# Kernel optimization log

Measured on AMD Instinct MI355X. Metric: run time of the kernel, lower is better.

Reference implementation:

```python
import jax, jax.numpy as jnp
import numpy as np

B, S, H = 2, 1024, 2048
HQ, HKV, D = 16, 4, 128
E, K, CAP = 32, 4, 512
IM, SIM = 512, 1024
EPS = 1e-6
THETA = 1.0e6
T = B * S


def setup_inputs() -> dict:
    key = jax.random.key(0)
    ks = jax.random.split(key, 16)
    r = lambda i, shape, s=0.02: jax.random.normal(ks[i], shape, dtype=jnp.float32) * s
    return {
        "hidden_states": jax.random.normal(ks[0], (T, H), dtype=jnp.float32),
        "positions": jnp.tile(jnp.arange(S, dtype=jnp.int32), B),
        "ln1_w": jnp.ones((H,), jnp.float32),
        "ln2_w": jnp.ones((H,), jnp.float32),
        "wq": r(1, (H, HQ * D)),
        "wk": r(2, (H, HKV * D)),
        "wv": r(3, (H, HKV * D)),
        "wo": r(4, (HQ * D, H)),
        "qn_w": jnp.ones((D,), jnp.float32),
        "kn_w": jnp.ones((D,), jnp.float32),
        "gate_w": r(5, (H, E), 0.05),
        "expert_bias": r(6, (E,), 0.1),
        "w_gate_e": r(7, (E, H, IM)),
        "w_up_e": r(8, (E, H, IM)),
        "w_down_e": r(9, (E, IM, H)),
        "ws_gate": r(10, (H, SIM)),
        "ws_up": r(11, (H, SIM)),
        "ws_down": r(12, (SIM, H)),
    }


def _rms(x, w):
    return x * jax.lax.rsqrt(jnp.mean(x * x, axis=-1, keepdims=True) + EPS) * w


def _forward(hidden_states, positions, ln1_w, ln2_w, wq, wk, wv, wo, qn_w, kn_w,
             gate_w, expert_bias, w_gate_e, w_up_e, w_down_e, ws_gate, ws_up, ws_down):
    # --- attention block ---
    resid = hidden_states
    h = _rms(hidden_states, ln1_w)
    q = (h @ wq).reshape(T, HQ, D)
    k = (h @ wk).reshape(T, HKV, D)
    v = (h @ wv).reshape(T, HKV, D)
    q = _rms(q, qn_w)  # per-head qk-norm
    k = _rms(k, kn_w)
    # neox-style RoPE over full head_dim
    inv = 1.0 / (THETA ** (jnp.arange(0, D, 2, dtype=jnp.float32) / D))
    fr = positions.astype(jnp.float32)[:, None] * inv  # [T, D/2]
    cos, sin = jnp.cos(fr)[:, None, :], jnp.sin(fr)[:, None, :]
    def rope(x):
        x1, x2 = jnp.split(x, 2, axis=-1)
        return jnp.concatenate([x1 * cos - x2 * sin, x2 * cos + x1 * sin], axis=-1)
    q, k = rope(q), rope(k)
    qb = q.reshape(B, S, HQ, D)
    kb = jnp.repeat(k.reshape(B, S, HKV, D), HQ // HKV, axis=2)  # GQA expand
    vb = jnp.repeat(v.reshape(B, S, HKV, D), HQ // HKV, axis=2)
    sc = jnp.einsum('bqhd,bkhd->bhqk', qb, kb) * (D ** -0.5)
    causal = jnp.tril(jnp.ones((S, S), dtype=bool))
    sc = jnp.where(causal, sc, jnp.float32(-1e30))
    p = jax.nn.softmax(sc, axis=-1)
    ao = jnp.einsum('bhqk,bkhd->bqhd', p, vb).reshape(T, HQ * D)
    h = ao @ wo + resid
    resid = h
    h = _rms(h, ln2_w)
    # --- shared experts (dense MLP) ---
    shared = (jax.nn.silu(h @ ws_gate) * (h @ ws_up)) @ ws_down
    # --- sigmoid router with correction bias (bias only for selection) ---
    scores = jax.nn.sigmoid(h @ gate_w)          # [T, E]
    _, idx = jax.lax.top_k(scores + expert_bias, K)
    w = jnp.take_along_axis(scores, idx, axis=-1)
    w = w / jnp.sum(w, axis=-1, keepdims=True)   # renormalize top-k probs
    # --- capacity-based dispatch / grouped GEMM / combine ---
    flat_e = idx.reshape(-1)                     # [T*K]
    flat_t = jnp.repeat(jnp.arange(T), K)
    flat_w = w.reshape(-1)
    order = jnp.argsort(flat_e)                  # stable sort by expert
    se, st, sw = flat_e[order], flat_t[order], flat_w[order]
    counts = jnp.bincount(flat_e, length=E)
    starts = jnp.concatenate([jnp.zeros((1,), counts.dtype), jnp.cumsum(counts)[:-1]])
    pos = jnp.arange(T * K) - starts[se]         # slot within expert
    valid = pos < CAP                            # capacity guard (never trips in practice)
    posc = jnp.minimum(pos, CAP - 1)
    xbuf = jnp.zeros((E, CAP, H), h.dtype).at[se, posc].add(
        jnp.where(valid[:, None], h[st], 0.0))   # [E, CAP, H]
    inter = jax.nn.silu(jnp.einsum('ech,ehi->eci', xbuf, w_gate_e)) \
            * jnp.einsum('ech,ehi->eci', xbuf, w_up_e)
    obuf = jnp.einsum('eci,eih->ech', inter, w_down_e)
    y = obuf[se, posc] * jnp.where(valid, sw, 0.0)[:, None]
    moe = jnp.zeros((T, H), h.dtype).at[st].add(y)
    return resid + moe + shared


def reference(hidden_states, positions, ln1_w, ln2_w, wq, wk, wv, wo, qn_w, kn_w,
              gate_w, expert_bias, w_gate_e, w_up_e, w_down_e, ws_gate, ws_up, ws_down):
    return _forward(hidden_states, positions, ln1_w, ln2_w, wq, wk, wv, wo, qn_w, kn_w,
                    gate_w, expert_bias, w_gate_e, w_up_e, w_down_e, ws_gate, ws_up, ws_down)
```

## Files before the change

### kernel.cpp

```cpp
#include <hip/hip_runtime.h>
#include <stdint.h>

typedef unsigned short u16;
typedef unsigned short bf16u;
typedef unsigned int u32;
typedef _Float16 f16;
typedef __attribute__((ext_vector_type(8))) short bf16x8;
typedef __attribute__((ext_vector_type(8))) _Float16 f16x8;
typedef __attribute__((ext_vector_type(4))) float f32x4;

#define T_N 2048
#define H_N 2048
#define S_N 1024
#define B_N 2
#define HQ_N 16
#define HKV_N 4
#define D_N 128
#define E_N 32
#define K_TOP 4
#define CAP_N 512
#define IM_N 512
#define SIM_N 1024
#define QD_N 2048
#define KD_N 512
#define QKV_N 3072
#define NFLAT (T_N*K_TOP)
#define RGRP 128
#define NGRP (NFLAT/RGRP)

#define SC_H1   1024.0f
#define SC_W    512.0f
#define SC_QK   2048.0f
#define SC_P    4096.0f
#define SC_V    2048.0f
#define OSC_QKV (1.0f/524288.0f)
#define OSC_OPJ (1.0f/1048576.0f)

__device__ __forceinline__ float bf2f(bf16u x){ return __uint_as_float(((u32)x)<<16); }
__device__ __forceinline__ bf16u f2bf(float f){
  u32 u = __float_as_uint(f);
  u32 r = (u + 0x7FFFu + ((u>>16)&1u)) >> 16;
  return (bf16u)r;
}
__device__ __forceinline__ u32 pkbf(float a, float b){
  u32 ua = __float_as_uint(a), ub = __float_as_uint(b);
  u32 ra = (ua + 0x7FFFu + ((ua>>16)&1u)) >> 16;
  u32 rb = (ub + 0x7FFFu + ((ub>>16)&1u)) & 0xFFFF0000u;
  return ra | rb;
}
__device__ __forceinline__ void split2h(float x, u16& h, u16& l){
  f16 hh = (f16)x;
  f16 ll = (f16)(x - (float)hh);
  h = __builtin_bit_cast(u16, hh);
  l = __builtin_bit_cast(u16, ll);
}
__device__ __forceinline__ f32x4 mfma16b(bf16x8 a, bf16x8 b, f32x4 c){
  return __builtin_amdgcn_mfma_f32_16x16x32_bf16(a,b,c,0,0,0);
}
__device__ __forceinline__ f32x4 mfma16h(f16x8 a, f16x8 b, f32x4 c){
  return __builtin_amdgcn_mfma_f32_16x16x32_f16(a,b,c,0,0,0);
}
__device__ __forceinline__ void gl_lds16(const void* g, void* l){
  __builtin_amdgcn_global_load_lds((const __attribute__((address_space(1))) u32*)g,
                                   (__attribute__((address_space(3))) u32*)l, 16, 0, 0);
}
__device__ __forceinline__ int xcd_swz(int lin, int nwg){
  int cpx = nwg >> 3;
  return (lin & 7)*cpx + (lin >> 3);
}

__global__ __launch_bounds__(256) void transpose_f32(const float* __restrict__ in,
                                                     float* __restrict__ out, int R, int C){
  __shared__ float tile[32][33];
  int rb = blockIdx.x*32, cb = blockIdx.y*32;
  int tx = threadIdx.x, ty = threadIdx.y;
  #pragma unroll
  for (int kk=0;kk<4;kk++)
    tile[ty+kk*8][tx] = in[(size_t)(rb+ty+kk*8)*C + cb + tx];
  __syncthreads();
  #pragma unroll
  for (int kk=0;kk<4;kk++)
    out[(size_t)(cb+ty+kk*8)*R + rb + tx] = tile[tx][ty+kk*8];
}

__global__ __launch_bounds__(256) void transpose_cvt_g(const float* __restrict__ in,
                                                       bf16u* __restrict__ out, int R, int C){
  __shared__ float tile[64*64];
  size_t zo = (size_t)blockIdx.z * R * C;
  int rb = blockIdx.x*64, cb = blockIdx.y*64;
  int tid = threadIdx.x, wave = tid>>6, lane = tid&63;
  #pragma unroll
  for (int p=0;p<4;p++){
    int r = p*16 + wave*4 + (lane>>4);
    const float* src = in + zo + (size_t)(rb + r)*C + cb + (lane&15)*4;
    gl_lds16(src, &tile[(p*16 + wave*4)*64]);
  }
  __syncthreads();
  int c = tid>>2, rq = (tid&3)*16;
  u16 tmp[16];
  #pragma unroll
  for (int j=0;j<16;j++) tmp[j] = f2bf(tile[(rq+j)*64 + c]);
  uint4 w0, w1;
  w0.x=(u32)tmp[0]|((u32)tmp[1]<<16);  w0.y=(u32)tmp[2]|((u32)tmp[3]<<16);
  w0.z=(u32)tmp[4]|((u32)tmp[5]<<16);  w0.w=(u32)tmp[6]|((u32)tmp[7]<<16);
  w1.x=(u32)tmp[8]|((u32)tmp[9]<<16);  w1.y=(u32)tmp[10]|((u32)tmp[11]<<16);
  w1.z=(u32)tmp[12]|((u32)tmp[13]<<16); w1.w=(u32)tmp[14]|((u32)tmp[15]<<16);
  bf16u* dst = out + zo + (size_t)(cb+c)*R + rb + rq;
  *(uint4*)dst = w0;
  *(uint4*)(dst+8) = w1;
}

__global__ __launch_bounds__(256) void transpose_split16_g(const float* __restrict__ in,
                                                           u16* __restrict__ oh,
                                                           u16* __restrict__ ol,
                                                           int R, int C, float scale){
  __shared__ float tile[64*64];
  int rb = blockIdx.x*64, cb = blockIdx.y*64;
  int tid = threadIdx.x, wave = tid>>6, lane = tid&63;
  #pragma unroll
  for (int p=0;p<4;p++){
    int r = p*16 + wave*4 + (lane>>4);
    const float* src = in + (size_t)(rb + r)*C + cb + (lane&15)*4;
    gl_lds16(src, &tile[(p*16 + wave*4)*64]);
  }
  __syncthreads();
  int c = tid>>2, rq = (tid&3)*16;
  u16 th[16], tl[16];
  #pragma unroll
  for (int j=0;j<16;j++) split2h(tile[(rq+j)*64 + c]*scale, th[j], tl[j]);
  uint4 h0, h1, l0, l1;
  h0.x=(u32)th[0]|((u32)th[1]<<16);  h0.y=(u32)th[2]|((u32)th[3]<<16);
  h0.z=(u32)th[4]|((u32)th[5]<<16);  h0.w=(u32)th[6]|((u32)th[7]<<16);
  h1.x=(u32)th[8]|((u32)th[9]<<16);  h1.y=(u32)th[10]|((u32)th[11]<<16);
  h1.z=(u32)th[12]|((u32)th[13]<<16); h1.w=(u32)th[14]|((u32)th[15]<<16);
  l0.x=(u32)tl[0]|((u32)tl[1]<<16);  l0.y=(u32)tl[2]|((u32)tl[3]<<16);
  l0.z=(u32)tl[4]|((u32)tl[5]<<16);  l0.w=(u32)tl[6]|((u32)tl[7]<<16);
  l1.x=(u32)tl[8]|((u32)tl[9]<<16);  l1.y=(u32)tl[10]|((u32)tl[11]<<16);
  l1.z=(u32)tl[12]|((u32)tl[13]<<16); l1.w=(u32)tl[14]|((u32)tl[15]<<16);
  size_t o = (size_t)(cb+c)*R + rb + rq;
  *(uint4*)(oh + o) = h0; *(uint4*)(oh + o + 8) = h1;
  *(uint4*)(ol + o) = l0; *(uint4*)(ol + o + 8) = l1;
}

__global__ __launch_bounds__(256) void rmsnorm_bf16(const float* __restrict__ x,
                                                    const float* __restrict__ w,
                                                    bf16u* __restrict__ y){
  int row = blockIdx.x; int t = threadIdx.x;
  const float4* x4 = (const float4*)(x + (size_t)row*H_N);
  float4 a = x4[2*t], b = x4[2*t+1];
  float ss = a.x*a.x+a.y*a.y+a.z*a.z+a.w*a.w + b.x*b.x+b.y*b.y+b.z*b.z+b.w*b.w;
  #pragma unroll
  for (int m=32;m>=1;m>>=1) ss += __shfl_xor(ss,m,64);
  __shared__ float red[4];
  if ((t&63)==0) red[t>>6]=ss;
  __syncthreads();
  float scale = rsqrtf((red[0]+red[1]+red[2]+red[3])*(1.0f/H_N) + 1e-6f);
  const float4* w4 = (const float4*)w;
  float4 wa = w4[2*t], wb = w4[2*t+1];
  uint4 pk;
  pk.x = pkbf(a.x*scale*wa.x, a.y*scale*wa.y);
  pk.y = pkbf(a.z*scale*wa.z, a.w*scale*wa.w);
  pk.z = pkbf(b.x*scale*wb.x, b.y*scale*wb.y);
  pk.w = pkbf(b.z*scale*wb.z, b.w*scale*wb.w);
  ((uint4*)(y + (size_t)row*H_N))[t] = pk;
}

__global__ __launch_bounds__(256) void rmsnorm_f16split(const float* __restrict__ x,
                                                        const float* __restrict__ w,
                                                        u16* __restrict__ yh,
                                                        u16* __restrict__ yl){
  int row = blockIdx.x; int t = threadIdx.x;
  const float4* x4 = (const float4*)(x + (size_t)row*H_N);
  float4 a = x4[2*t], b = x4[2*t+1];
  float ss = a.x*a.x+a.y*a.y+a.z*a.z+a.w*a.w + b.x*b.x+b.y*b.y+b.z*b.z+b.w*b.w;
  #pragma unroll
  for (int m=32;m>=1;m>>=1) ss += __shfl_xor(ss,m,64);
  __shared__ float red[4];
  if ((t&63)==0) red[t>>6]=ss;
  __syncthreads();
  float scale = rsqrtf((red[0]+red[1]+red[2]+red[3])*(1.0f/H_N) + 1e-6f) * SC_H1;
  const float4* w4 = (const float4*)w;
  float4 wa = w4[2*t], wb = w4[2*t+1];
  float o[8] = {a.x*scale*wa.x, a.y*scale*wa.y, a.z*scale*wa.z, a.w*scale*wa.w,
                b.x*scale*wb.x, b.y*scale*wb.y, b.z*scale*wb.z, b.w*scale*wb.w};
  u16 hh[8], ll[8];
  #pragma unroll
  for (int j=0;j<8;j++) split2h(o[j], hh[j], ll[j]);
  uint4 pk, pl;
  pk.x = (u32)hh[0]|((u32)hh[1]<<16); pk.y = (u32)hh[2]|((u32)hh[3]<<16);
  pk.z = (u32)hh[4]|((u32)hh[5]<<16); pk.w = (u32)hh[6]|((u32)hh[7]<<16);
  pl.x = (u32)ll[0]|((u32)ll[1]<<16); pl.y = (u32)ll[2]|((u32)ll[3]<<16);
  pl.z = (u32)ll[4]|((u32)ll[5]<<16); pl.w = (u32)ll[6]|((u32)ll[7]<<16);
  ((uint4*)(yh + (size_t)row*H_N))[t] = pk;
  ((uint4*)(yl + (size_t)row*H_N))[t] = pl;
}

__global__ void qknorm_rope_split(const float* __restrict__ qkv,
                                  const float* __restrict__ qw, const float* __restrict__ kw,
                                  const int* __restrict__ positions,
                                  u16* __restrict__ qho, u16* __restrict__ qlo,
                                  u16* __restrict__ kho, u16* __restrict__ klo){
  int t = blockIdx.x; int hy = blockIdx.y; int l = threadIdx.x;
  const float* p; const float* w; u16 *oh, *ol; size_t obase;
  if (hy < HQ_N){
    p = qkv + (size_t)t*QKV_N + hy*D_N; w = qw;
    oh = qho; ol = qlo; obase = (size_t)t*QD_N + hy*D_N;
  } else {
    p = qkv + (size_t)t*QKV_N + QD_N + (hy-HQ_N)*D_N; w = kw;
    oh = kho; ol = klo; obase = (size_t)t*KD_N + (hy-HQ_N)*D_N;
  }
  float x0 = p[l], x1 = p[l+64];
  float ss = x0*x0 + x1*x1;
  #pragma unroll
  for (int m=32;m>=1;m>>=1) ss += __shfl_xor(ss,m,64);
  float scale = rsqrtf(ss*(1.0f/D_N)+1e-6f);
  x0 *= scale*w[l]; x1 *= scale*w[l+64];
  double freq = exp2(-(double)l * (19.931568569324174/64.0));
  double fr = (double)positions[t] * freq;
  double sd, cd; sincos(fr, &sd, &cd);
  float r0 = (float)((double)x0*cd - (double)x1*sd) * SC_QK;
  float r1 = (float)((double)x1*cd + (double)x0*sd) * SC_QK;
  u16 hh, ll;
  split2h(r0, hh, ll); oh[obase+l] = hh; ol[obase+l] = ll;
  split2h(r1, hh, ll); oh[obase+l+64] = hh; ol[obase+l+64] = ll;
}

__global__ __launch_bounds__(256) void transpose_v_split(const float* __restrict__ in,
                                                         u16* __restrict__ oh,
                                                         u16* __restrict__ ol){
  __shared__ u16 th[32][33];
  __shared__ u16 tl[32][33];
  int z = blockIdx.z; int b = z >> 2, kvh = z & 3;
  const float* ip = in + (size_t)b*S_N*QKV_N + QD_N + KD_N + kvh*D_N;
  size_t ob = (size_t)z*D_N*S_N;
  int sb = blockIdx.x*32, db = blockIdx.y*32;
  int tx=threadIdx.x, ty=threadIdx.y;
  #pragma unroll
  for (int kk=0;kk<4;kk++){
    float x = ip[(size_t)(sb+ty+kk*8)*QKV_N + db+tx] * SC_V;
    u16 hh, ll; split2h(x, hh, ll);
    th[ty+kk*8][tx] = hh; tl[ty+kk*8][tx] = ll;
  }
  __syncthreads();
  #pragma unroll
  for (int kk=0;kk<4;kk++){
    size_t idx = ob + (size_t)(db+ty+kk*8)*S_N + sb+tx;
    oh[idx] = th[tx][ty+kk*8];
    ol[idx] = tl[tx][ty+kk*8];
  }
}

template<int MODE, bool SPLIT>
__global__ __launch_bounds__(512) void gemm_bt8(
    const u16* __restrict__ A, const u16* __restrict__ Al,
    const u16* __restrict__ B0g, const u16* __restrict__ B0lg,
    const u16* __restrict__ B1g,
    void* __restrict__ Cout, const float* __restrict__ resid, float oscale,
    int N, int Kd)
{
  constexpr bool DUAL = (MODE==2);
  __shared__ u16 As[2][128*32];
  __shared__ u16 Bs0[2][128*32];
  __shared__ u16 Asl[SPLIT?2:1][SPLIT?128*32:8];
  __shared__ u16 Bs0l[SPLIT?2:1][SPLIT?128*32:8];
  __shared__ u16 Bs1[DUAL?2:1][DUAL?128*32:8];

  int tid = threadIdx.x;
  int wave = tid>>6, lane = tid&63, l15 = lane&15, lg = lane>>4;
  int nwgx = gridDim.x;
  int lin = blockIdx.y*nwgx + blockIdx.x;
  int swz = xcd_swz(lin, nwgx*gridDim.y);
  int mBase = (swz % nwgx)*128;
  int nBase = (swz / nwgx)*128;

  int r = tid>>2, c = (tid&3)*8;
  size_t aOff = (size_t)(mBase + r)*Kd + c;
  size_t bOff = (size_t)(nBase + r)*Kd + c;

  auto STAGE = [&](int buf, int kt){
    size_t ko = (size_t)kt*32;
    gl_lds16(A + aOff + ko, &As[buf][tid*8]);
    gl_lds16(B0g + bOff + ko, &Bs0[buf][tid*8]);
    if constexpr (SPLIT){
      gl_lds16(Al + aOff + ko, &Asl[buf][tid*8]);
      gl_lds16(B0lg + bOff + ko, &Bs0l[buf][tid*8]);
    }
    if constexpr (DUAL){
      gl_lds16(B1g + bOff + ko, &Bs1[buf][tid*8]);
    }
  };

  f32x4 zero4 = {0.f,0.f,0.f,0.f};
  f32x4 acc0[2][4];
  f32x4 acc1[DUAL?2:1][DUAL?4:1];
  #pragma unroll
  for (int mi=0;mi<2;mi++)
    #pragma unroll
    for (int ni=0;ni<4;ni++){
      acc0[mi][ni] = zero4;
      if constexpr (DUAL) acc1[mi][ni] = zero4;
    }

  int wm = wave>>1, wn = wave&1;
  int nK = Kd >> 5;
  STAGE(0, 0);
  __syncthreads();
  for (int kt=0; kt<nK; kt++){
    int cur = kt&1;
    if (kt+1 < nK) STAGE(cur^1, kt+1);
    if constexpr (SPLIT){
      f16x8 af[2], afl[2];
      #pragma unroll
      for (int mi=0;mi<2;mi++){
        af[mi]  = *(const f16x8*)&As [cur][(wm*32 + mi*16 + l15)*32 + lg*8];
        afl[mi] = *(const f16x8*)&Asl[cur][(wm*32 + mi*16 + l15)*32 + lg*8];
      }
      #pragma unroll
      for (int ni=0;ni<4;ni++){
        f16x8 b0  = *(const f16x8*)&Bs0 [cur][(wn*64 + ni*16 + l15)*32 + lg*8];
        f16x8 b0l = *(const f16x8*)&Bs0l[cur][(wn*64 + ni*16 + l15)*32 + lg*8];
        #pragma unroll
        for (int mi=0;mi<2;mi++){
          acc0[mi][ni] = mfma16h(af[mi], b0, acc0[mi][ni]);
          acc0[mi][ni] = mfma16h(af[mi], b0l, acc0[mi][ni]);
          acc0[mi][ni] = mfma16h(afl[mi], b0, acc0[mi][ni]);
        }
      }
    } else {
      bf16x8 af[2];
      #pragma unroll
      for (int mi=0;mi<2;mi++)
        af[mi] = *(const bf16x8*)&As[cur][(wm*32 + mi*16 + l15)*32 + lg*8];
      #pragma unroll
      for (int ni=0;ni<4;ni++){
        bf16x8 b0 = *(const bf16x8*)&Bs0[cur][(wn*64 + ni*16 + l15)*32 + lg*8];
        #pragma unroll
        for (int mi=0;mi<2;mi++) acc0[mi][ni] = mfma16b(af[mi], b0, acc0[mi][ni]);
        if constexpr (DUAL){
          bf16x8 b1 = *(const bf16x8*)&Bs1[cur][(wn*64 + ni*16 + l15)*32 + lg*8];
          #pragma unroll
          for (int mi=0;mi<2;mi++) acc1[mi][ni] = mfma16b(af[mi], b1, acc1[mi][ni]);
        }
      }
    }
    __syncthreads();
  }

  #pragma unroll
  for (int mi=0;mi<2;mi++){
    #pragma unroll
    for (int ni=0;ni<4;ni++){
      #pragma unroll
      for (int i=0;i<4;i++){
        int rloc = wm*32 + mi*16 + 4*lg + i;
        int col  = nBase + wn*64 + ni*16 + l15;
        float v = acc0[mi][ni][i];
        if constexpr (MODE==1){
          size_t idx = (size_t)(mBase + rloc)*N + col;
          ((float*)Cout)[idx] = v*oscale + (resid ? resid[idx] : 0.0f);
        } else {
          float u = acc1[mi][ni][i];
          float sv = v/(1.0f+__expf(-v))*u;
          ((bf16u*)Cout)[(size_t)(mBase + rloc)*N + col] = f2bf(sv);
        }
      }
    }
  }
}

__global__ __launch_bounds__(512) void moe_gu8w(
    const u16* __restrict__ A,
    const u16* __restrict__ B0g,
    const u16* __restrict__ B1g,
    bf16u* __restrict__ Out,
    const int* __restrict__ starts, const int* __restrict__ counts,
    const int* __restrict__ perm)
{
  __shared__ u16 As[2][128*32];
  __shared__ u16 Bs0[2][128*32];
  __shared__ u16 Bs1[2][128*32];

  int nwgx = gridDim.x, nwgy = gridDim.y;
  int lin = (blockIdx.z*nwgy + blockIdx.y)*nwgx + blockIdx.x;
  int swz = xcd_swz(lin, nwgx*nwgy*gridDim.z);
  int bx = swz % nwgx; swz /= nwgx;
  int by = swz % nwgy;
  int e  = swz / nwgy;

  int cnt = counts[e]; cnt = cnt < CAP_N ? cnt : CAP_N;
  int mBase = bx*128;
  int rows = cnt - mBase;
  if (rows <= 0) return;
  if (rows > 128) rows = 128;
  int slotBase = starts[e] + mBase;
  int nBase = by*128;
  const u16* Bp0 = B0g + (size_t)e*IM_N*H_N;
  const u16* Bp1 = B1g + (size_t)e*IM_N*H_N;

  int tid = threadIdx.x, wave = tid>>6, lane = tid&63, l15 = lane&15, lg = lane>>4;
  int r = tid>>2, c = (tid&3)*8;
  int rr = (r < rows) ? r : 0;
  size_t aOff = (size_t)perm[slotBase + rr]*H_N + c;
  size_t bOff = (size_t)(nBase + r)*H_N + c;

  auto STAGE = [&](int buf, int kt){
    size_t ko = (size_t)kt*32;
    gl_lds16(A + aOff + ko, &As[buf][tid*8]);
    gl_lds16(Bp0 + bOff + ko, &Bs0[buf][tid*8]);
    gl_lds16(Bp1 + bOff + ko, &Bs1[buf][tid*8]);
  };

  f32x4 zero4 = {0.f,0.f,0.f,0.f};
  f32x4 acc0[2][4], acc1[2][4];
  #pragma unroll
  for (int mi=0;mi<2;mi++)
    #pragma unroll
    for (int ni=0;ni<4;ni++){ acc0[mi][ni]=zero4; acc1[mi][ni]=zero4; }

  int wm = wave>>1, wn = wave&1;
  STAGE(0, 0);
  __syncthreads();
  int nK = H_N >> 5;
  for (int kt=0; kt<nK; kt++){
    int cur = kt&1;
    if (kt+1 < nK) STAGE(cur^1, kt+1);
    bf16x8 af[2];
    #pragma unroll
    for (int mi=0;mi<2;mi++)
      af[mi] = *(const bf16x8*)&As[cur][(wm*32 + mi*16 + l15)*32 + lg*8];
    #pragma unroll
    for (int ni=0;ni<4;ni++){
      bf16x8 b0 = *(const bf16x8*)&Bs0[cur][(wn*64 + ni*16 + l15)*32 + lg*8];
      bf16x8 b1 = *(const bf16x8*)&Bs1[cur][(wn*64 + ni*16 + l15)*32 + lg*8];
      #pragma unroll
      for (int mi=0;mi<2;mi++){
        acc0[mi][ni] = mfma16b(af[mi], b0, acc0[mi][ni]);
        acc1[mi][ni] = mfma16b(af[mi], b1, acc1[mi][ni]);
      }
    }
    __syncthreads();
  }

  #pragma unroll
  for (int mi=0;mi<2;mi++){
    #pragma unroll
    for (int ni=0;ni<4;ni++){
      #pragma unroll
      for (int i=0;i<4;i++){
        int rloc = wm*32 + mi*16 + 4*lg + i;
        if (rloc < rows){
          float v = acc0[mi][ni][i];
          float u = acc1[mi][ni][i];
          float sv = v/(1.0f+__expf(-v))*u;
          Out[(size_t)(slotBase + rloc)*IM_N + nBase + wn*64 + ni*16 + l15] = f2bf(sv);
        }
      }
    }
  }
}

__global__ __launch_bounds__(512) void moe_down8w(
    const u16* __restrict__ A,
    const u16* __restrict__ B0g,
    bf16u* __restrict__ Out,
    const int* __restrict__ starts, const int* __restrict__ counts)
{
  __shared__ u16 As[2][128*32];
  __shared__ u16 Bs0[2][128*32];

  int nwgx = gridDim.x, nwgy = gridDim.y;
  int lin = (blockIdx.z*nwgy + blockIdx.y)*nwgx + blockIdx.x;
  int swz = xcd_swz(lin, nwgx*nwgy*gridDim.z);
  int bx = swz % nwgx; swz /= nwgx;
  int by = swz % nwgy;
  int e  = swz / nwgy;

  int cnt = counts[e]; cnt = cnt < CAP_N ? cnt : CAP_N;
  int mBase = bx*128;
  int rows = cnt - mBase;
  if (rows <= 0) return;
  if (rows > 128) rows = 128;
  int slotBase = starts[e] + mBase;
  int nBase = by*128;
  const u16* Bp0 = B0g + (size_t)e*H_N*IM_N;

  int tid = threadIdx.x, wave = tid>>6, lane = tid&63, l15 = lane&15, lg = lane>>4;
  int r = tid>>2, c = (tid&3)*8;
  int rr = (r < rows) ? r : 0;
  size_t aOff = (size_t)(slotBase + rr)*IM_N + c;
  size_t bOff = (size_t)(nBase + r)*IM_N + c;

  auto STAGE = [&](int buf, int kt){
    size_t ko = (size_t)kt*32;
    gl_lds16(A + aOff + ko, &As[buf][tid*8]);
    gl_lds16(Bp0 + bOff + ko, &Bs0[buf][tid*8]);
  };

  f32x4 zero4 = {0.f,0.f,0.f,0.f};
  f32x4 acc0[2][4];
  #pragma unroll
  for (int mi=0;mi<2;mi++)
    #pragma unroll
    for (int ni=0;ni<4;ni++) acc0[mi][ni]=zero4;

  int wm = wave>>1, wn = wave&1;
  STAGE(0, 0);
  __syncthreads();
  int nK = IM_N >> 5;
  for (int kt=0; kt<nK; kt++){
    int cur = kt&1;
    if (kt+1 < nK) STAGE(cur^1, kt+1);
    bf16x8 af[2];
    #pragma unroll
    for (int mi=0;mi<2;mi++)
      af[mi] = *(const bf16x8*)&As[cur][(wm*32 + mi*16 + l15)*32 + lg*8];
    #pragma unroll
    for (int ni=0;ni<4;ni++){
      bf16x8 b0 = *(const bf16x8*)&Bs0[cur][(wn*64 + ni*16 + l15)*32 + lg*8];
      #pragma unroll
      for (int mi=0;mi<2;mi++)
        acc0[mi][ni] = mfma16b(af[mi], b0, acc0[mi][ni]);
    }
    __syncthreads();
  }

  #pragma unroll
  for (int mi=0;mi<2;mi++){
    #pragma unroll
    for (int ni=0;ni<4;ni++){
      #pragma unroll
      for (int i=0;i<4;i++){
        int rloc = wm*32 + mi*16 + 4*lg + i;
        if (rloc < rows)
          Out[(size_t)(slotBase + rloc)*H_N + nBase + wn*64 + ni*16 + l15] = f2bf(acc0[mi][ni][i]);
      }
    }
  }
}

__global__ __launch_bounds__(512) void attn_kernel(
    const u16* __restrict__ qh, const u16* __restrict__ ql,
    const u16* __restrict__ kh, const u16* __restrict__ kl,
    const u16* __restrict__ vth, const u16* __restrict__ vtl,
    u16* __restrict__ aoh, u16* __restrict__ aol)
{
  int bx = blockIdx.x;
  int bh = blockIdx.y;
  int b = bh >> 4, h = bh & 15, kvh = h >> 2;
  int tid = threadIdx.x, wave = tid>>6, lane = tid&63, l15 = lane&15, lg = lane>>4;

  __shared__ u16 Ksh[64*136];
  __shared__ u16 Ksl[64*136];
  __shared__ u16 Vsh[128*72];
  __shared__ u16 Vsl[128*72];
  __shared__ u16 Psh[8][16*72];
  __shared__ u16 Psl[8][16*72];

  int qtile = (wave < 4) ? bx : (15 - bx);
  int wl = wave & 3;
  int qrow0 = qtile*64 + wl*16;

  size_t qrow = (size_t)(b*S_N + qrow0 + l15)*QD_N + h*D_N;
  f16x8 qfh[4], qfl[4];
  #pragma unroll
  for (int ds=0; ds<4; ds++){
    qfh[ds] = *(const f16x8*)(qh + qrow + ds*32 + lg*8);
    qfl[ds] = *(const f16x8*)(ql + qrow + ds*32 + lg*8);
  }

  f32x4 zero4 = {0.f,0.f,0.f,0.f};
  f32x4 accO[8];
  #pragma unroll
  for (int dc=0; dc<8; dc++) accO[dc] = zero4;
  float mrun[4], lrun[4];
  #pragma unroll
  for (int i=0;i<4;i++){ mrun[i] = -3.0e38f; lrun[i] = 0.0f; }

  const float SC_S = 0.08838834764831845f * (1.0f/(SC_QK*SC_QK));
  int nkt = 16 - bx;
  for (int kt=0; kt<nkt; kt++){
    #pragma unroll
    for (int pp=0; pp<2; pp++){
      int r = pp*32 + (tid>>4), c = (tid&15)*8;
      size_t go = (size_t)(b*S_N + kt*64 + r)*KD_N + kvh*D_N + c;
      *(f16x8*)&Ksh[r*136 + c] = *(const f16x8*)(kh + go);
      *(f16x8*)&Ksl[r*136 + c] = *(const f16x8*)(kl + go);
    }
    #pragma unroll
    for (int pp=0; pp<2; pp++){
      int r = pp*64 + (tid>>3), c = (tid&7)*8;
      size_t go = ((size_t)(b*HKV_N + kvh)*D_N + r)*S_N + kt*64 + c;
      *(f16x8*)&Vsh[r*72 + c] = *(const f16x8*)(vth + go);
      *(f16x8*)&Vsl[r*72 + c] = *(const f16x8*)(vtl + go);
    }
    __syncthreads();

    bool active = (kt <= qtile);
    if (active){
      f32x4 sacc[4];
      #pragma unroll
      for (int kc=0;kc<4;kc++){
        sacc[kc] = zero4;
        #pragma unroll
        for (int ds=0; ds<4; ds++){
          f16x8 kfh = *(const f16x8*)&Ksh[(kc*16 + l15)*136 + ds*32 + lg*8];
          f16x8 kfl = *(const f16x8*)&Ksl[(kc*16 + l15)*136 + ds*32 + lg*8];
          sacc[kc] = mfma16h(qfh[ds], kfh, sacc[kc]);
          sacc[kc] = mfma16h(qfh[ds], kfl, sacc[kc]);
          sacc[kc] = mfma16h(qfl[ds], kfh, sacc[kc]);
        }
      }

      float pv[4][4];
      bool maskT = (kt == qtile);
      #pragma unroll
      for (int kc=0;kc<4;kc++)
        #pragma unroll
        for (int i=0;i<4;i++){
          float sv = sacc[kc][i] * SC_S;
          if (maskT){
            int kg = kt*64 + kc*16 + l15;
            int qg = qrow0 + 4*lg + i;
            if (kg > qg) sv = -3.0e38f;
          }
          pv[kc][i] = sv;
        }

      #pragma unroll
      for (int i=0;i<4;i++){
        float mx = fmaxf(fmaxf(pv[0][i],pv[1][i]),fmaxf(pv[2][i],pv[3][i]));
        #pragma unroll
        for (int mm=1; mm<16; mm<<=1) mx = fmaxf(mx, __shfl_xor(mx, mm, 64));
        float mnew = fmaxf(mrun[i], mx);
        float corr = exp2f((mrun[i]-mnew)*1.44269504f);
        float ps = 0.f;
        #pragma unroll
        for (int kc=0;kc<4;kc++){
          float p = exp2f((pv[kc][i]-mnew)*1.44269504f);
          pv[kc][i] = p; ps += p;
        }
        #pragma unroll
        for (int mm=1; mm<16; mm<<=1) ps += __shfl_xor(ps, mm, 64);
        lrun[i] = lrun[i]*corr + ps;
        mrun[i] = mnew;
        #pragma unroll
        for (int dc=0;dc<8;dc++) accO[dc][i] *= corr;
      }

      #pragma unroll
      for (int kc=0;kc<4;kc++)
        #pragma unroll
        for (int i=0;i<4;i++){
          u16 hh, ll; split2h(pv[kc][i]*SC_P, hh, ll);
          Psh[wave][(4*lg+i)*72 + kc*16 + l15] = hh;
          Psl[wave][(4*lg+i)*72 + kc*16 + l15] = ll;
        }
      asm volatile("s_waitcnt lgkmcnt(0)" ::: "memory");
      __builtin_amdgcn_sched_barrier(0);

      #pragma unroll
      for (int ks=0; ks<2; ks++){
        f16x8 pfh = *(const f16x8*)&Psh[wave][l15*72 + ks*32 + lg*8];
        f16x8 pfl = *(const f16x8*)&Psl[wave][l15*72 + ks*32 + lg*8];
        #pragma unroll
        for (int dc=0; dc<8; dc++){
          f16x8 vfh = *(const f16x8*)&Vsh[(dc*16 + l15)*72 + ks*32 + lg*8];
          f16x8 vfl = *(const f16x8*)&Vsl[(dc*16 + l15)*72 + ks*32 + lg*8];
          accO[dc] = mfma16h(pfh, vfh, accO[dc]);
          accO[dc] = mfma16h(pfh, vfl, accO[dc]);
          accO[dc] = mfma16h(pfl, vfh, accO[dc]);
        }
      }
    }
    __syncthreads();
  }

  #pragma unroll
  for (int i=0;i<4;i++){
    float inv = 1.0f / (4096.0f * lrun[i]);
    size_t orow = (size_t)(b*S_N + qrow0 + 4*lg + i)*QD_N + h*D_N;
    #pragma unroll
    for (int dc=0; dc<8; dc++){
      u16 hh, ll; split2h(accO[dc][i]*inv, hh, ll);
      aoh[orow + dc*16 + l15] = hh;
      aol[orow + dc*16 + l15] = ll;
    }
  }
}

__global__ __launch_bounds__(256) void router_kernel(
    const float* __restrict__ resid2, const float* __restrict__ ln2w,
    const float* __restrict__ gwT, const float* __restrict__ ebias,
    int* __restrict__ tkIdx, float* __restrict__ tkW, int* __restrict__ counts)
{
  int t = blockIdx.x, tid = threadIdx.x;
  __shared__ float xs[H_N];
  __shared__ float red[4];
  __shared__ float sc[E_N];
  const float4* x4 = (const float4*)(resid2 + (size_t)t*H_N);
  float4 a = x4[2*tid], b = x4[2*tid+1];
  float ss = a.x*a.x+a.y*a.y+a.z*a.z+a.w*a.w + b.x*b.x+b.y*b.y+b.z*b.z+b.w*b.w;
  #pragma unroll
  for (int m=32;m>=1;m>>=1) ss += __shfl_xor(ss,m,64);
  if ((tid&63)==0) red[tid>>6]=ss;
  __syncthreads();
  float scale = rsqrtf((red[0]+red[1]+red[2]+red[3])*(1.0f/H_N) + 1e-6f);
  const float4* w4 = (const float4*)ln2w;
  float4 wa = w4[2*tid], wb = w4[2*tid+1];
  xs[tid*8+0]=a.x*scale*wa.x; xs[tid*8+1]=a.y*scale*wa.y;
  xs[tid*8+2]=a.z*scale*wa.z; xs[tid*8+3]=a.w*scale*wa.w;
  xs[tid*8+4]=b.x*scale*wb.x; xs[tid*8+5]=b.y*scale*wb.y;
  xs[tid*8+6]=b.z*scale*wb.z; xs[tid*8+7]=b.w*scale*wb.w;
  __syncthreads();
  int wave = tid>>6, lane = tid&63;
  const float4* xv4 = (const float4*)xs;
  #pragma unroll
  for (int ei=0; ei<8; ei++){
    int e = wave*8 + ei;
    const float4* g4 = (const float4*)(gwT + (size_t)e*H_N);
    float acc = 0.f;
    #pragma unroll
    for (int it=0; it<8; it++){
      int idx = it*64 + lane;
      float4 g = g4[idx], xv = xv4[idx];
      acc += g.x*xv.x + g.y*xv.y + g.z*xv.z + g.w*xv.w;
    }
    #pragma unroll
    for (int m=32;m>=1;m>>=1) acc += __shfl_xor(acc,m,64);
    if (lane==0) sc[e] = 1.0f/(1.0f+__expf(-acc));
  }
  __syncthreads();
  if (tid==0){
    float sb[E_N];
    #pragma unroll
    for (int e2=0;e2<E_N;e2++) sb[e2] = sc[e2]+ebias[e2];
    int ch[4]; float wv[4]; float wsum=0.f;
    for (int j=0;j<4;j++){
      int best=0; float bv=-3.0e38f;
      for (int e2=0;e2<E_N;e2++) if (sb[e2] > bv){ bv=sb[e2]; best=e2; }
      ch[j]=best; wv[j]=sc[best]; wsum+=sc[best]; sb[best]=-3.0e38f;
    }
    float invs = 1.0f/wsum;
    for (int j=0;j<4;j++){
      tkIdx[t*4+j]=ch[j]; tkW[t*4+j]=wv[j]*invs;
      atomicAdd(&counts[ch[j]], 1);
    }
  }
}

__global__ void moe_count_kernel(const int* __restrict__ tki, int* __restrict__ G){
  __shared__ int cnt[E_N];
  int g = blockIdx.x, t = threadIdx.x;
  if (t < E_N) cnt[t] = 0;
  __syncthreads();
  atomicAdd(&cnt[tki[g*RGRP + t]], 1);
  __syncthreads();
  if (t < E_N) G[g*E_N + t] = cnt[t];
}

__global__ void moe_scan_kernel(const int* __restrict__ G, int* __restrict__ base,
                                int* __restrict__ starts){
  __shared__ int tot[E_N];
  int e = threadIdx.x;
  if (e < E_N){
    int run = 0;
    for (int g=0; g<NGRP; g++){ base[g*E_N+e] = run; run += G[g*E_N+e]; }
    tot[e] = run < CAP_N ? run : CAP_N;
  }
  __syncthreads();
  if (e==0){
    int run=0;
    for (int x=0; x<E_N; x++){ starts[x]=run; run+=tot[x]; }
  }
}

__global__ void moe_assign_kernel(const int* __restrict__ tki,
                                  const int* __restrict__ base, const int* __restrict__ starts,
                                  int* __restrict__ ptok, int* __restrict__ tok2slot){
  __shared__ int eL[RGRP];
  int g = blockIdx.x, t = threadIdx.x;
  int f = g*RGRP + t;
  int e = tki[f];
  eL[t] = e;
  __syncthreads();
  int r = 0;
  for (int j=0; j<RGRP; j++) r += ((j < t) && (eL[j]==e)) ? 1 : 0;
  int pos = base[g*E_N + e] + r;
  if (pos < CAP_N){
    int slot = starts[e] + pos;
    ptok[slot] = f >> 2;
    tok2slot[f] = slot;
  } else {
    tok2slot[f] = -1;
  }
}

__global__ __launch_bounds__(256) void moe_combine(const int* __restrict__ tok2slot,
                                                   const float* __restrict__ tkw,
                                                   const bf16u* __restrict__ obuf,
                                                   float* __restrict__ outp){
  int t = blockIdx.x;
  int c0 = threadIdx.x*8;
  float acc[8];
  float4* o4 = (float4*)(outp + (size_t)t*H_N + c0);
  float4 v0 = o4[0], v1 = o4[1];
  acc[0]=v0.x; acc[1]=v0.y; acc[2]=v0.z; acc[3]=v0.w;
  acc[4]=v1.x; acc[5]=v1.y; acc[6]=v1.z; acc[7]=v1.w;
  #pragma unroll
  for (int j=0;j<4;j++){
    int slot = tok2slot[t*4+j];
    if (slot >= 0){
      float w = tkw[t*4+j];
      bf16x8 ob = *(const bf16x8*)(obuf + (size_t)slot*H_N + c0);
      #pragma unroll
      for (int q=0;q<8;q++) acc[q] += w * bf2f((bf16u)ob[q]);
    }
  }
  v0.x=acc[0]; v0.y=acc[1]; v0.z=acc[2]; v0.w=acc[3];
  v1.x=acc[4]; v1.y=acc[5]; v1.z=acc[6]; v1.w=acc[7];
  o4[0]=v0; o4[1]=v1;
}

extern "C" void kernel_launch(void* const* d_in, const int* in_sizes, int n_in,
                              void* d_out, int out_size, void* d_ws, size_t ws_size,
                              hipStream_t stream) {
  (void)in_sizes; (void)n_in; (void)out_size; (void)ws_size;
  const float* hidden    = (const float*)d_in[0];
  const int*   positions = (const int*)d_in[1];
  const float* ln1w = (const float*)d_in[2];
  const float* ln2w = (const float*)d_in[3];
  const float* wq   = (const float*)d_in[4];
  const float* wk   = (const float*)d_in[5];
  const float* wv   = (const float*)d_in[6];
  const float* wo   = (const float*)d_in[7];
  const float* qnw  = (const float*)d_in[8];
  const float* knw  = (const float*)d_in[9];
  const float* gatew= (const float*)d_in[10];
  const float* ebias= (const float*)d_in[11];
  const float* wge  = (const float*)d_in[12];
  const float* wue  = (const float*)d_in[13];
  const float* wde  = (const float*)d_in[14];
  const float* wsg  = (const float*)d_in[15];
  const float* wsu  = (const float*)d_in[16];
  const float* wsd  = (const float*)d_in[17];
  float* outp = (float*)d_out;

  char* wsb = (char*)d_ws;
  size_t off = 0;
  auto take = [&](size_t bytes)->char*{
    char* p = wsb + off; off += (bytes + 255) & ~(size_t)255; return p;
  };
  u16* qkvTh = (u16*)take(3072ull*2048*2);
  u16* qkvTl = (u16*)take(3072ull*2048*2);
  u16* woTh = (u16*)take(2048ull*2048*2);
  u16* woTl = (u16*)take(2048ull*2048*2);
  u16* wsgT = (u16*)take(1024ull*2048*2);
  u16* wsuT = (u16*)take(1024ull*2048*2);
  u16* wsdT = (u16*)take(2048ull*1024*2);
  u16* wgeT = (u16*)take(32ull*512*2048*2);
  u16* wueT = (u16*)take(32ull*512*2048*2);
  u16* wdeT = (u16*)take(32ull*2048*512*2);
  float* gwT = (float*)take(32ull*2048*4);
  u16* h1h  = (u16*)take((size_t)T_N*H_N*2);
  u16* h1l  = (u16*)take((size_t)T_N*H_N*2);
  float* qkv32 = (float*)take((size_t)T_N*QKV_N*4);
  u16* qHh  = (u16*)take((size_t)T_N*QD_N*2);
  u16* qHl  = (u16*)take((size_t)T_N*QD_N*2);
  u16* kHh  = (u16*)take((size_t)T_N*KD_N*2);
  u16* kHl  = (u16*)take((size_t)T_N*KD_N*2);
  u16* vtHh = (u16*)take((size_t)T_N*KD_N*2);
  u16* vtHl = (u16*)take((size_t)T_N*KD_N*2);
  u16* aoh  = (u16*)take((size_t)T_N*QD_N*2);
  u16* aol  = (u16*)take((size_t)T_N*QD_N*2);
  float* resid2=(float*)take((size_t)T_N*H_N*4);
  u16* h2   = (u16*)take((size_t)T_N*H_N*2);
  u16* interS=(u16*)take((size_t)T_N*SIM_N*2);
  u16* minter=(u16*)take((size_t)NFLAT*IM_N*2);
  bf16u* obuf = (bf16u*)take((size_t)NFLAT*H_N*2);
  int*   tki  = (int*)take((size_t)NFLAT*4);
  float* tkw  = (float*)take((size_t)NFLAT*4);
  int*   counts=(int*)take(E_N*4);
  int*   Gcnt = (int*)take((size_t)NGRP*E_N*4);
  int*   Gbase= (int*)take((size_t)NGRP*E_N*4);
  int*   starts=(int*)take(E_N*4);
  int*   ptok = (int*)take((size_t)NFLAT*4);
  int*   tok2slot = (int*)take((size_t)NFLAT*4);

  hipMemsetAsync(counts, 0, 256, stream);

  dim3 tb(32,8);
  transpose_split16_g<<<dim3(32,32), 256, 0, stream>>>(wq, qkvTh, qkvTl, 2048, 2048, SC_W);
  transpose_split16_g<<<dim3(32,8),  256, 0, stream>>>(wk, qkvTh + 2048ull*2048, qkvTl + 2048ull*2048, 2048, 512, SC_W);
  transpose_split16_g<<<dim3(32,8),  256, 0, stream>>>(wv, qkvTh + 2560ull*2048, qkvTl + 2560ull*2048, 2048, 512, SC_W);
  transpose_split16_g<<<dim3(32,32), 256, 0, stream>>>(wo, woTh, woTl, 2048, 2048, SC_W);
  transpose_cvt_g<<<dim3(32,16,1), 256, 0, stream>>>(wsg, wsgT, 2048, 1024);
  transpose_cvt_g<<<dim3(32,16,1), 256, 0, stream>>>(wsu, wsuT, 2048, 1024);
  transpose_cvt_g<<<dim3(16,32,1), 256, 0, stream>>>(wsd, wsdT, 1024, 2048);
  transpose_cvt_g<<<dim3(32,8,32), 256, 0, stream>>>(wge, wgeT, 2048, 512);
  transpose_cvt_g<<<dim3(32,8,32), 256, 0, stream>>>(wue, wueT, 2048, 512);
  transpose_cvt_g<<<dim3(8,32,32), 256, 0, stream>>>(wde, wdeT, 512, 2048);
  transpose_f32<<<dim3(64,1,1), tb, 0, stream>>>(gatew, gwT, 2048, 32);

  rmsnorm_f16split<<<T_N, 256, 0, stream>>>(hidden, ln1w, h1h, h1l);
  gemm_bt8<1,true><<<dim3(16,24), 512, 0, stream>>>(h1h, h1l, qkvTh, qkvTl, nullptr, qkv32, nullptr, OSC_QKV, QKV_N, H_N);
  qknorm_rope_split<<<dim3(T_N,20), 64, 0, stream>>>(qkv32, qnw, knw, positions, qHh, qHl, kHh, kHl);
  transpose_v_split<<<dim3(32,4,8), tb, 0, stream>>>(qkv32, vtHh, vtHl);
  attn_kernel<<<dim3(8,32), 512, 0, stream>>>(qHh, qHl, kHh, kHl, vtHh, vtHl, aoh, aol);
  gemm_bt8<1,true><<<dim3(16,16), 512, 0, stream>>>(aoh, aol, woTh, woTl, nullptr, resid2, hidden, OSC_OPJ, H_N, QD_N);
  rmsnorm_bf16<<<T_N, 256, 0, stream>>>(resid2, ln2w, (bf16u*)h2);
  gemm_bt8<2,false><<<dim3(16,8), 512, 0, stream>>>(h2, nullptr, wsgT, nullptr, wsuT, interS, nullptr, 1.0f, SIM_N, H_N);
  gemm_bt8<1,false><<<dim3(16,16), 512, 0, stream>>>(interS, nullptr, wsdT, nullptr, nullptr, outp, resid2, 1.0f, H_N, SIM_N);
  router_kernel<<<T_N, 256, 0, stream>>>(resid2, ln2w, gwT, ebias, tki, tkw, counts);
  moe_count_kernel<<<NGRP, RGRP, 0, stream>>>(tki, Gcnt);
  moe_scan_kernel<<<1, 64, 0, stream>>>(Gcnt, Gbase, starts);
  moe_assign_kernel<<<NGRP, RGRP, 0, stream>>>(tki, Gbase, starts, ptok, tok2slot);
  moe_gu8w<<<dim3(4,4,32), 512, 0, stream>>>(h2, wgeT, wueT, minter, starts, counts, ptok);
  moe_down8w<<<dim3(4,16,32), 512, 0, stream>>>(minter, wdeT, obuf, starts, counts);
  moe_combine<<<T_N, 256, 0, stream>>>(tok2slot, tkw, obuf, outp);
}
```

Baseline: 790.0 us.

## Use partial vmcnt waits and raw barriers to overlap next-tile loads in GEMMs

In the three GEMM kernels, the blanket __syncthreads is replaced by explicit s_waitcnt vmcnt(N) waits. Each wave now waits only for the current tile's global-to-LDS loads while the next tile's prefetch stays in flight, followed by raw s_barrier calls and sched_barrier fences. The MFMA loops are also wrapped in s_setprio(1) so waves doing math get issue priority. This aims to overlap the next-tile prefetch with compute instead of draining all memory ops each iteration. It relies on the vmcnt counts matching the exact number of loads issued per stage, so a wrong count could produce a race.

```diff
diff --git a/kernel.cpp b/kernel.cpp
--- a/kernel.cpp
+++ b/kernel.cpp
@@ -64,6 +64,13 @@
   __builtin_amdgcn_global_load_lds((const __attribute__((address_space(1))) u32*)g,
                                    (__attribute__((address_space(3))) u32*)l, 16, 0, 0);
 }
+template<int N> __device__ __forceinline__ void waitv(){
+  if constexpr (N==0) asm volatile("s_waitcnt vmcnt(0)" ::: "memory");
+  else if constexpr (N==2) asm volatile("s_waitcnt vmcnt(2)" ::: "memory");
+  else if constexpr (N==3) asm volatile("s_waitcnt vmcnt(3)" ::: "memory");
+  else if constexpr (N==4) asm volatile("s_waitcnt vmcnt(4)" ::: "memory");
+  __builtin_amdgcn_sched_barrier(0);
+}
 __device__ __forceinline__ int xcd_swz(int lin, int nwg){
   int cpx = nwg >> 3;
   return (lin & 7)*cpx + (lin >> 3);
@@ -259,6 +266,7 @@
     int N, int Kd)
 {
   constexpr bool DUAL = (MODE==2);
+  constexpr int LD = SPLIT ? 4 : (DUAL ? 3 : 2);
   __shared__ u16 As[2][128*32];
   __shared__ u16 Bs0[2][128*32];
   __shared__ u16 Asl[SPLIT?2:1][SPLIT?128*32:8];
@@ -304,10 +312,12 @@
   int wm = wave>>1, wn = wave&1;
   int nK = Kd >> 5;
   STAGE(0, 0);
-  __syncthreads();
   for (int kt=0; kt<nK; kt++){
     int cur = kt&1;
-    if (kt+1 < nK) STAGE(cur^1, kt+1);
+    if (kt+1 < nK){ STAGE(cur^1, kt+1); waitv<LD>(); }
+    else waitv<0>();
+    __builtin_amdgcn_s_barrier();
+    __builtin_amdgcn_sched_barrier(0);
     if constexpr (SPLIT){
       f16x8 af[2], afl[2];
       #pragma unroll
@@ -315,6 +325,7 @@
         af[mi]  = *(const f16x8*)&As [cur][(wm*32 + mi*16 + l15)*32 + lg*8];
         afl[mi] = *(const f16x8*)&Asl[cur][(wm*32 + mi*16 + l15)*32 + lg*8];
       }
+      __builtin_amdgcn_s_setprio(1);
       #pragma unroll
       for (int ni=0;ni<4;ni++){
         f16x8 b0  = *(const f16x8*)&Bs0 [cur][(wn*64 + ni*16 + l15)*32 + lg*8];
@@ -326,11 +337,13 @@
           acc0[mi][ni] = mfma16h(afl[mi], b0, acc0[mi][ni]);
         }
       }
+      __builtin_amdgcn_s_setprio(0);
     } else {
       bf16x8 af[2];
       #pragma unroll
       for (int mi=0;mi<2;mi++)
         af[mi] = *(const bf16x8*)&As[cur][(wm*32 + mi*16 + l15)*32 + lg*8];
+      __builtin_amdgcn_s_setprio(1);
       #pragma unroll
       for (int ni=0;ni<4;ni++){
         bf16x8 b0 = *(const bf16x8*)&Bs0[cur][(wn*64 + ni*16 + l15)*32 + lg*8];
@@ -342,8 +355,11 @@
           for (int mi=0;mi<2;mi++) acc1[mi][ni] = mfma16b(af[mi], b1, acc1[mi][ni]);
         }
       }
-    }
-    __syncthreads();
+      __builtin_amdgcn_s_setprio(0);
+    }
+    asm volatile("s_waitcnt lgkmcnt(0)" ::: "memory");
+    __builtin_amdgcn_sched_barrier(0);
+    __builtin_amdgcn_s_barrier();
   }
 
   #pragma unroll
@@ -419,15 +435,18 @@
 
   int wm = wave>>1, wn = wave&1;
   STAGE(0, 0);
-  __syncthreads();
   int nK = H_N >> 5;
   for (int kt=0; kt<nK; kt++){
     int cur = kt&1;
-    if (kt+1 < nK) STAGE(cur^1, kt+1);
+    if (kt+1 < nK){ STAGE(cur^1, kt+1); waitv<3>(); }
+    else waitv<0>();
+    __builtin_amdgcn_s_barrier();
+    __builtin_amdgcn_sched_barrier(0);
     bf16x8 af[2];
     #pragma unroll
     for (int mi=0;mi<2;mi++)
       af[mi] = *(const bf16x8*)&As[cur][(wm*32 + mi*16 + l15)*32 + lg*8];
+    __builtin_amdgcn_s_setprio(1);
     #pragma unroll
     for (int ni=0;ni<4;ni++){
       bf16x8 b0 = *(const bf16x8*)&Bs0[cur][(wn*64 + ni*16 + l15)*32 + lg*8];
@@ -438,7 +457,10 @@
         acc1[mi][ni] = mfma16b(af[mi], b1, acc1[mi][ni]);
       }
     }
-    __syncthreads();
+    __builtin_amdgcn_s_setprio(0);
+    asm volatile("s_waitcnt lgkmcnt(0)" ::: "memory");
+    __builtin_amdgcn_sched_barrier(0);
+    __builtin_amdgcn_s_barrier();
   }
 
   #pragma unroll
@@ -505,15 +527,18 @@
 
   int wm = wave>>1, wn = wave&1;
   STAGE(0, 0);
-  __syncthreads();
   int nK = IM_N >> 5;
   for (int kt=0; kt<nK; kt++){
     int cur = kt&1;
-    if (kt+1 < nK) STAGE(cur^1, kt+1);
+    if (kt+1 < nK){ STAGE(cur^1, kt+1); waitv<2>(); }
+    else waitv<0>();
+    __builtin_amdgcn_s_barrier();
+    __builtin_amdgcn_sched_barrier(0);
     bf16x8 af[2];
     #pragma unroll
     for (int mi=0;mi<2;mi++)
       af[mi] = *(const bf16x8*)&As[cur][(wm*32 + mi*16 + l15)*32 + lg*8];
+    __builtin_amdgcn_s_setprio(1);
     #pragma unroll
     for (int ni=0;ni<4;ni++){
       bf16x8 b0 = *(const bf16x8*)&Bs0[cur][(wn*64 + ni*16 + l15)*32 + lg*8];
@@ -521,7 +546,10 @@
       for (int mi=0;mi<2;mi++)
         acc0[mi][ni] = mfma16b(af[mi], b0, acc0[mi][ni]);
     }
-    __syncthreads();
+    __builtin_amdgcn_s_setprio(0);
+    asm volatile("s_waitcnt lgkmcnt(0)" ::: "memory");
+    __builtin_amdgcn_sched_barrier(0);
+    __builtin_amdgcn_s_barrier();
   }
 
   #pragma unroll
```

Result: no change. 790.9 us (+0.1%).
